# Kernel optimization log

Hardware: AMD Instinct MI355X
Metric: run time of the kernel (lower is better)

## Reference

```python
import jax, jax.numpy as jnp
from jax import lax
import numpy as np

NUM_LABELS = 48
BATCH, SEQ_LEN = 512, 1024


def setup_inputs() -> dict:
    key = jax.random.key(0)
    k1, k2, k3, k4, k5 = jax.random.split(key, 5)
    emissions = jax.random.normal(k1, (BATCH, SEQ_LEN, NUM_LABELS), dtype=jnp.float32)
    labels = jax.random.randint(k2, (BATCH, SEQ_LEN), 0, NUM_LABELS, dtype=jnp.int32)
    mask = jnp.ones((BATCH, SEQ_LEN), dtype=jnp.int32)
    transitions = jax.random.normal(k3, (NUM_LABELS, NUM_LABELS), dtype=jnp.float32)
    start_transitions = jax.random.normal(k4, (NUM_LABELS,), dtype=jnp.float32)
    end_transitions = jax.random.normal(k5, (NUM_LABELS,), dtype=jnp.float32)
    return {
        "emissions": emissions,
        "labels": labels,
        "mask": mask,
        "transitions": transitions,
        "start_transitions": start_transitions,
        "end_transitions": end_transitions,
    }


def _gold_score(emissions, labels, mask, transitions, start_transitions, end_transitions):
    maskf = mask.astype(emissions.dtype)
    # emissions gathered at gold labels: (B, T)
    emit = jnp.take_along_axis(emissions, labels[..., None], axis=2)[..., 0]
    # NOTE: original indexes transitions[labels_t, labels_{t-1}] (cur, prev)
    trans = transitions[labels[:, 1:], labels[:, :-1]]  # (B, T-1)
    lengths = jnp.sum(mask, axis=1) - 1  # index of last real token
    last_labels = jnp.take_along_axis(labels, lengths[:, None], axis=1)[:, 0]
    score = (start_transitions[labels[:, 0]] + emit[:, 0]
             + jnp.sum((emit[:, 1:] + trans) * maskf[:, 1:], axis=1)
             + end_transitions[last_labels])
    return score  # (B,)


def _forward_algorithm(emissions, mask, transitions, start_transitions, end_transitions):
    # carry: alpha scores (B, L)
    score0 = start_transitions[None, :] + emissions[:, 0]

    def step(score, xs):
        emit_t, mask_t = xs  # (B, L), (B,)
        # logsumexp over previous label i of score[b,i] + transitions[i,j]
        next_score = jax.nn.logsumexp(score[:, :, None] + transitions[None, :, :], axis=1) + emit_t
        score = jnp.where(mask_t[:, None].astype(bool), next_score, score)
        return score, None

    xs = (jnp.moveaxis(emissions[:, 1:], 1, 0), jnp.moveaxis(mask[:, 1:], 1, 0))
    score, _ = lax.scan(step, score0, xs)
    return jax.nn.logsumexp(score + end_transitions[None, :], axis=1)  # (B,)


def reference(emissions, labels, mask, transitions, start_transitions, end_transitions):
    gold = _gold_score(emissions, labels, mask, transitions, start_transitions, end_transitions)
    fwd = _forward_algorithm(emissions, mask, transitions, start_transitions, end_transitions)
    return jnp.mean(fwd - gold)
```

## Files before the change

### kernel.cpp

```cpp
#include <hip/hip_runtime.h>

constexpr int NL    = 48;
constexpr int SEQ   = 1024;
constexpr int BATCH = 512;

__device__ __forceinline__ float lane_bcast(float v, int lane) {
    return __int_as_float(__builtin_amdgcn_readlane(__float_as_int(v), lane));
}

#define CRF_STEP(T_, SLOT_, RN_) do {                                         \
    float ee_ = __expf(embuf[SLOT_]);                                         \
    int   mt_ = mbuf[SLOT_];                                                  \
    int   tn_ = (T_) + 8; if (tn_ > SEQ - 1) tn_ = SEQ - 1;                   \
    embuf[SLOT_] = em[tn_ * NL + jc];                                         \
    mbuf[SLOT_]  = mk[tn_];                                                   \
    float sv_[NL];                                                            \
    _Pragma("unroll")                                                         \
    for (int i_ = 0; i_ < NL; ++i_) sv_[i_] = lane_bcast(v, i_);              \
    float rm_ = 1.0f;                                                         \
    if (RN_) {                                                                \
        unsigned um_ = __float_as_uint(sv_[0]);                               \
        _Pragma("unroll")                                                     \
        for (int i_ = 1; i_ < NL; ++i_) {                                     \
            unsigned u2_ = __float_as_uint(sv_[i_]);                          \
            um_ = (um_ > u2_) ? um_ : u2_;                                    \
        }                                                                     \
        float m_ = __uint_as_float(um_);                                      \
        rm_ = __builtin_amdgcn_rcpf(m_);                                      \
        S += __logf(m_);                                                      \
    }                                                                         \
    float a0_ = 0.f, a1_ = 0.f, a2_ = 0.f, a3_ = 0.f;                         \
    _Pragma("unroll")                                                         \
    for (int i_ = 0; i_ < NL; i_ += 4) {                                      \
        a0_ = fmaf(sv_[i_ + 0], Ec[i_ + 0], a0_);                             \
        a1_ = fmaf(sv_[i_ + 1], Ec[i_ + 1], a1_);                             \
        a2_ = fmaf(sv_[i_ + 2], Ec[i_ + 2], a2_);                             \
        a3_ = fmaf(sv_[i_ + 3], Ec[i_ + 3], a3_);                             \
    }                                                                         \
    float acc_ = (a0_ + a1_) + (a2_ + a3_);                                   \
    v = (mt_ ? acc_ * ee_ : v) * rm_;                                         \
} while (0)

__global__ __launch_bounds__(128)
__attribute__((amdgpu_waves_per_eu(1, 1)))
void crf_fused(
    const float* __restrict__ emissions, const int* __restrict__ labels,
    const int* __restrict__ mask, const float* __restrict__ trans,
    const float* __restrict__ startt, const float* __restrict__ endt,
    float* __restrict__ gold_out, float* __restrict__ fwd_out)
{
    const int b   = blockIdx.x;
    const int tid = threadIdx.x;
    const float* em = emissions + (size_t)b * SEQ * NL;
    const int*   mk = mask + b * SEQ;

    if (tid < 64) {
        const int  j   = tid;
        const bool act = (j < NL);
        const int  jc  = act ? j : NL - 1;

        float Ec[NL];
        #pragma unroll
        for (int i = 0; i < NL; ++i) Ec[i] = __expf(trans[i * NL + jc]);

        float s0 = act ? (startt[jc] + em[jc]) : -3.0e38f;
        float m0 = s0;
        #pragma unroll
        for (int o = 32; o; o >>= 1) m0 = fmaxf(m0, __shfl_xor(m0, o));
        float v = act ? __expf(s0 - m0) : 0.0f;
        float S = m0;

        float embuf[8]; int mbuf[8];
        #pragma unroll
        for (int t = 1; t <= 8; ++t) { embuf[t & 7] = em[t * NL + jc]; mbuf[t & 7] = mk[t]; }

        CRF_STEP(1, 1, 0); CRF_STEP(2, 2, 0); CRF_STEP(3, 3, 0); CRF_STEP(4, 4, 0);
        CRF_STEP(5, 5, 1); CRF_STEP(6, 6, 0); CRF_STEP(7, 7, 0);

        for (int tb = 8; tb <= SEQ - 8; tb += 8) {
            CRF_STEP(tb + 0, 0, 1);
            CRF_STEP(tb + 1, 1, 0); CRF_STEP(tb + 2, 2, 0); CRF_STEP(tb + 3, 3, 0);
            CRF_STEP(tb + 4, 4, 1);
            CRF_STEP(tb + 5, 5, 0); CRF_STEP(tb + 6, 6, 0); CRF_STEP(tb + 7, 7, 0);
        }

        float w = act ? v * __expf(endt[jc]) : 0.0f;
        #pragma unroll
        for (int o = 32; o; o >>= 1) w += __shfl_xor(w, o);
        if (j == 0) fwd_out[b] = S + __logf(w);
    } else {
        const int l = tid - 64;
        const int* lb = labels + b * SEQ;

        float part = 0.0f; int mcnt = 0;
        for (int t = l; t < SEQ; t += 64) {
            int lt = lb[t];
            int mt = mk[t];
            mcnt += mt;
            if (t == 0) {
                part += startt[lt] + em[lt];
            } else {
                float e  = em[t * NL + lt];
                float tr = trans[lt * NL + lb[t - 1]];
                if (mt) part += e + tr;
            }
        }
        #pragma unroll
        for (int o = 32; o; o >>= 1) {
            part += __shfl_xor(part, o);
            mcnt += __shfl_xor(mcnt, o);
        }
        if (l == 0) {
            int len = mcnt - 1;
            gold_out[b] = part + endt[lb[len]];
        }
    }
}

__global__ __launch_bounds__(64) void crf_reduce(
    const float* __restrict__ gold, const float* __restrict__ fwd,
    float* __restrict__ out)
{
    const int l = threadIdx.x;
    float s = 0.0f;
    for (int bIdx = l; bIdx < BATCH; bIdx += 64) s += fwd[bIdx] - gold[bIdx];
    #pragma unroll
    for (int o = 32; o; o >>= 1) s += __shfl_xor(s, o);
    if (l == 0) out[0] = s * (1.0f / (float)BATCH);
}

extern "C" void kernel_launch(void* const* d_in, const int* in_sizes, int n_in,
                              void* d_out, int out_size, void* d_ws, size_t ws_size,
                              hipStream_t stream) {
    const float* emissions = (const float*)d_in[0];
    const int*   labels    = (const int*)d_in[1];
    const int*   mask      = (const int*)d_in[2];
    const float* trans     = (const float*)d_in[3];
    const float* startt    = (const float*)d_in[4];
    const float* endt      = (const float*)d_in[5];
    float*       out       = (float*)d_out;
    float*       wsf       = (float*)d_ws;

    crf_fused<<<BATCH, 128, 0, stream>>>(emissions, labels, mask, trans, startt, endt,
                                         wsf, wsf + BATCH);
    crf_reduce<<<1, 64, 0, stream>>>(wsf, wsf + BATCH, out);
}
```

Before: 356.2 us.

## Pack alpha into bf16 pairs to halve readlane broadcasts per CRF step

Each step now rounds every lane's alpha to bf16, pairs neighbouring lanes with a DPP swap, and packs two bf16 values into one 32-bit word. Only 24 readlanes are needed per step instead of 48, and the values are unpacked into floats in scalar/vector ALU before the FMAs. The aim is to shorten the serial readlane chain on the recurrence's critical path. In exchange, the carried probabilities lose precision to bf16 across 1024 steps, which may affect accuracy, and the extra shift and mask operations add ALU work.

```diff
diff --git a/kernel.cpp b/kernel.cpp
--- a/kernel.cpp
+++ b/kernel.cpp
@@ -3,10 +3,6 @@
 constexpr int NL    = 48;
 constexpr int SEQ   = 1024;
 constexpr int BATCH = 512;
-
-__device__ __forceinline__ float lane_bcast(float v, int lane) {
-    return __int_as_float(__builtin_amdgcn_readlane(__float_as_int(v), lane));
-}
 
 #define CRF_STEP(T_, SLOT_, RN_) do {                                         \
     float ee_ = __expf(embuf[SLOT_]);                                         \
@@ -14,28 +10,42 @@
     int   tn_ = (T_) + 8; if (tn_ > SEQ - 1) tn_ = SEQ - 1;                   \
     embuf[SLOT_] = em[tn_ * NL + jc];                                         \
     mbuf[SLOT_]  = mk[tn_];                                                   \
-    float sv_[NL];                                                            \
+    int ar_ = __float_as_int(v) + 0x8000;          \
+    int br_ = __builtin_amdgcn_update_dpp(0, ar_, 0xB1, 0xF, 0xF, false);     \
+    int xl_ = odd ? br_ : ar_;                   \
+    int xh_ = odd ? ar_ : br_;                   \
+    int pk_ = (int)(((unsigned)xl_ >> 16) | ((unsigned)xh_ & 0xFFFF0000u));   \
+    int sp_[24];                                                              \
     _Pragma("unroll")                                                         \
-    for (int i_ = 0; i_ < NL; ++i_) sv_[i_] = lane_bcast(v, i_);              \
+    for (int p_ = 0; p_ < 24; ++p_)                                           \
+        sp_[p_] = __builtin_amdgcn_readlane(pk_, 2 * p_);                     \
     float rm_ = 1.0f;                                                         \
     if (RN_) {                                                                \
-        unsigned um_ = __float_as_uint(sv_[0]);                               \
+        unsigned mh_ = 0u, ml_ = 0u;                                          \
         _Pragma("unroll")                                                     \
-        for (int i_ = 1; i_ < NL; ++i_) {                                     \
-            unsigned u2_ = __float_as_uint(sv_[i_]);                          \
-            um_ = (um_ > u2_) ? um_ : u2_;                                    \
+        for (int p_ = 0; p_ < 24; ++p_) {                                     \
+            unsigned u_ = (unsigned)sp_[p_];                                  \
+            mh_ = (mh_ > u_) ? mh_ : u_;                                      \
+            unsigned l_ = u_ << 16;                                           \
+            ml_ = (ml_ > l_) ? ml_ : l_;                                      \
         }                                                                     \
-        float m_ = __uint_as_float(um_);                                      \
+        mh_ &= 0xFFFF0000u;                                                   \
+        unsigned mb_ = (mh_ > ml_) ? mh_ : ml_;                               \
+        float m_ = __uint_as_float(mb_);                                      \
         rm_ = __builtin_amdgcn_rcpf(m_);                                      \
         S += __logf(m_);                                                      \
     }                                                                         \
     float a0_ = 0.f, a1_ = 0.f, a2_ = 0.f, a3_ = 0.f;                         \
     _Pragma("unroll")                                                         \
-    for (int i_ = 0; i_ < NL; i_ += 4) {                                      \
-        a0_ = fmaf(sv_[i_ + 0], Ec[i_ + 0], a0_);                             \
-        a1_ = fmaf(sv_[i_ + 1], Ec[i_ + 1], a1_);                             \
-        a2_ = fmaf(sv_[i_ + 2], Ec[i_ + 2], a2_);                             \
-        a3_ = fmaf(sv_[i_ + 3], Ec[i_ + 3], a3_);                             \
+    for (int p_ = 0; p_ < 24; p_ += 2) {                                      \
+        float l0_ = __int_as_float((int)((unsigned)sp_[p_]     << 16));       \
+        float h0_ = __int_as_float((int)((unsigned)sp_[p_]     & 0xFFFF0000u));\
+        float l1_ = __int_as_float((int)((unsigned)sp_[p_ + 1] << 16));       \
+        float h1_ = __int_as_float((int)((unsigned)sp_[p_ + 1] & 0xFFFF0000u));\
+        a0_ = fmaf(l0_, Ec[2 * p_ + 0], a0_);                                 \
+        a1_ = fmaf(h0_, Ec[2 * p_ + 1], a1_);                                 \
+        a2_ = fmaf(l1_, Ec[2 * p_ + 2], a2_);                                 \
+        a3_ = fmaf(h1_, Ec[2 * p_ + 3], a3_);                                 \
     }                                                                         \
     float acc_ = (a0_ + a1_) + (a2_ + a3_);                                   \
     v = (mt_ ? acc_ * ee_ : v) * rm_;                                         \
@@ -58,6 +68,7 @@
         const int  j   = tid;
         const bool act = (j < NL);
         const int  jc  = act ? j : NL - 1;
+        const bool odd = (j & 1);
 
         float Ec[NL];
         #pragma unroll
```

Measured after the change: 412.3 us. +15.7%, slower.

## Interleave two batch sequences per wavefront to expose ILP in the CRF recurrence

Applied to the files above, without the earlier changes.

Each block now runs the forward recurrence for two batch elements (b and b+BATCH/2) inside one wavefront. The two independent chains are interleaved at each step: readlane broadcasts, max-renormalisation and FMAs for both are grouped in chunks of eight. The grid is halved to BATCH/2 blocks, and the gold-score wave loops over both sequences. The aim is to hide readlane and FMA latency on the serial dependency chain, at the cost of half as many concurrently active waves, more instructions per wave and higher register pressure.

```diff
diff --git a/kernel.cpp b/kernel.cpp
--- a/kernel.cpp
+++ b/kernel.cpp
@@ -8,37 +8,56 @@
     return __int_as_float(__builtin_amdgcn_readlane(__float_as_int(v), lane));
 }
 
-#define CRF_STEP(T_, SLOT_, RN_) do {                                         \
-    float ee_ = __expf(embuf[SLOT_]);                                         \
-    int   mt_ = mbuf[SLOT_];                                                  \
+#define CRF_STEP2(T_, SLOT_, RN_) do {                                        \
+    float eeA_ = __expf(embufA[SLOT_]);                                       \
+    float eeB_ = __expf(embufB[SLOT_]);                                       \
+    int   mtA_ = mbufA[SLOT_], mtB_ = mbufB[SLOT_];                           \
     int   tn_ = (T_) + 8; if (tn_ > SEQ - 1) tn_ = SEQ - 1;                   \
-    embuf[SLOT_] = em[tn_ * NL + jc];                                         \
-    mbuf[SLOT_]  = mk[tn_];                                                   \
-    float sv_[NL];                                                            \
+    embufA[SLOT_] = emA[tn_ * NL + jc];  mbufA[SLOT_] = mkA[tn_];             \
+    embufB[SLOT_] = emB[tn_ * NL + jc];  mbufB[SLOT_] = mkB[tn_];             \
+    float a0_=0.f,a1_=0.f,a2_=0.f,a3_=0.f;                                    \
+    float b0_=0.f,b1_=0.f,b2_=0.f,b3_=0.f;                                    \
+    unsigned umA_ = 0u, umB_ = 0u;                                            \
     _Pragma("unroll")                                                         \
-    for (int i_ = 0; i_ < NL; ++i_) sv_[i_] = lane_bcast(v, i_);              \
-    float rm_ = 1.0f;                                                         \
+    for (int g_ = 0; g_ < NL; g_ += 8) {                                      \
+        float sA_[8], sB_[8];                                                 \
+        _Pragma("unroll")                                                     \
+        for (int k_ = 0; k_ < 8; ++k_) {                                      \
+            sA_[k_] = lane_bcast(vA, g_ + k_);                                \
+            sB_[k_] = lane_bcast(vB, g_ + k_);                                \
+        }                                                                     \
+        if (RN_) {                                                            \
+            _Pragma("unroll")                                                 \
+            for (int k_ = 0; k_ < 8; ++k_) {                                  \
+                unsigned uA_ = __float_as_uint(sA_[k_]);                      \
+                umA_ = (umA_ > uA_) ? umA_ : uA_;                             \
+                unsigned uB_ = __float_as_uint(sB_[k_]);                      \
+                umB_ = (umB_ > uB_) ? umB_ : uB_;                             \
+            }                                                                 \
+        }                                                                     \
+        _Pragma("unroll")                                                     \
+        for (int k_ = 0; k_ < 8; k_ += 4) {                                   \
+            a0_ = fmaf(sA_[k_+0], Ec[g_+k_+0], a0_);                          \
+            b0_ = fmaf(sB_[k_+0], Ec[g_+k_+0], b0_);                          \
+            a1_ = fmaf(sA_[k_+1], Ec[g_+k_+1], a1_);                          \
+            b1_ = fmaf(sB_[k_+1], Ec[g_+k_+1], b1_);                          \
+            a2_ = fmaf(sA_[k_+2], Ec[g_+k_+2], a2_);                          \
+            b2_ = fmaf(sB_[k_+2], Ec[g_+k_+2], b2_);                          \
+            a3_ = fmaf(sA_[k_+3], Ec[g_+k_+3], a3_);                          \
+            b3_ = fmaf(sB_[k_+3], Ec[g_+k_+3], b3_);                          \
+        }                                                                     \
+    }                                                                         \
+    float rmA_ = 1.0f, rmB_ = 1.0f;                                           \
     if (RN_) {                                                                \
-        unsigned um_ = __float_as_uint(sv_[0]);                               \
-        _Pragma("unroll")                                                     \
-        for (int i_ = 1; i_ < NL; ++i_) {                                     \
-            unsigned u2_ = __float_as_uint(sv_[i_]);                          \
-            um_ = (um_ > u2_) ? um_ : u2_;                                    \
-        }                                                                     \
-        float m_ = __uint_as_float(um_);                                      \
-        rm_ = __builtin_amdgcn_rcpf(m_);                                      \
-        S += __logf(m_);                                                      \
+        float mA_ = __uint_as_float(umA_);                                    \
+        float mB_ = __uint_as_float(umB_);                                    \
+        rmA_ = __builtin_amdgcn_rcpf(mA_);  SA += __logf(mA_);                \
+        rmB_ = __builtin_amdgcn_rcpf(mB_);  SB += __logf(mB_);                \
     }                                                                         \
-    float a0_ = 0.f, a1_ = 0.f, a2_ = 0.f, a3_ = 0.f;                         \
-    _Pragma("unroll")                                                         \
-    for (int i_ = 0; i_ < NL; i_ += 4) {                                      \
-        a0_ = fmaf(sv_[i_ + 0], Ec[i_ + 0], a0_);                             \
-        a1_ = fmaf(sv_[i_ + 1], Ec[i_ + 1], a1_);                             \
-        a2_ = fmaf(sv_[i_ + 2], Ec[i_ + 2], a2_);                             \
-        a3_ = fmaf(sv_[i_ + 3], Ec[i_ + 3], a3_);                             \
-    }                                                                         \
-    float acc_ = (a0_ + a1_) + (a2_ + a3_);                                   \
-    v = (mt_ ? acc_ * ee_ : v) * rm_;                                         \
+    float accA_ = (a0_ + a1_) + (a2_ + a3_);                                  \
+    float accB_ = (b0_ + b1_) + (b2_ + b3_);                                  \
+    vA = (mtA_ ? accA_ * eeA_ : vA) * rmA_;                                   \
+    vB = (mtB_ ? accB_ * eeB_ : vB) * rmB_;                                   \
 } while (0)
 
 __global__ __launch_bounds__(128)
@@ -49,70 +68,97 @@
     const float* __restrict__ startt, const float* __restrict__ endt,
     float* __restrict__ gold_out, float* __restrict__ fwd_out)
 {
-    const int b   = blockIdx.x;
+    const int bA  = blockIdx.x;
+    const int bB  = blockIdx.x + (BATCH / 2);
     const int tid = threadIdx.x;
-    const float* em = emissions + (size_t)b * SEQ * NL;
-    const int*   mk = mask + b * SEQ;
 
     if (tid < 64) {
         const int  j   = tid;
         const bool act = (j < NL);
         const int  jc  = act ? j : NL - 1;
 
+        const float* emA = emissions + (size_t)bA * SEQ * NL;
+        const float* emB = emissions + (size_t)bB * SEQ * NL;
+        const int*   mkA = mask + bA * SEQ;
+        const int*   mkB = mask + bB * SEQ;
+
         float Ec[NL];
         #pragma unroll
         for (int i = 0; i < NL; ++i) Ec[i] = __expf(trans[i * NL + jc]);
 
-        float s0 = act ? (startt[jc] + em[jc]) : -3.0e38f;
-        float m0 = s0;
+        float st_ = act ? startt[jc] : 0.0f;
+        float s0A = act ? (st_ + emA[jc]) : -3.0e38f;
+        float s0B = act ? (st_ + emB[jc]) : -3.0e38f;
+        float m0A = s0A, m0B = s0B;
         #pragma unroll
-        for (int o = 32; o; o >>= 1) m0 = fmaxf(m0, __shfl_xor(m0, o));
-        float v = act ? __expf(s0 - m0) : 0.0f;
-        float S = m0;
+        for (int o = 32; o; o >>= 1) {
+            m0A = fmaxf(m0A, __shfl_xor(m0A, o));
+            m0B = fmaxf(m0B, __shfl_xor(m0B, o));
+        }
+        float vA = act ? __expf(s0A - m0A) : 0.0f;
+        float vB = act ? __expf(s0B - m0B) : 0.0f;
+        float SA = m0A, SB = m0B;
 
-        float embuf[8]; int mbuf[8];
+        float embufA[8], embufB[8]; int mbufA[8], mbufB[8];
         #pragma unroll
-        for (int t = 1; t <= 8; ++t) { embuf[t & 7] = em[t * NL + jc]; mbuf[t & 7] = mk[t]; }
+        for (int t = 1; t <= 8; ++t) {
+            embufA[t & 7] = emA[t * NL + jc];  mbufA[t & 7] = mkA[t];
+            embufB[t & 7] = emB[t * NL + jc];  mbufB[t & 7] = mkB[t];
+        }
 
-        CRF_STEP(1, 1, 0); CRF_STEP(2, 2, 0); CRF_STEP(3, 3, 0); CRF_STEP(4, 4, 0);
-        CRF_STEP(5, 5, 1); CRF_STEP(6, 6, 0); CRF_STEP(7, 7, 0);
+        CRF_STEP2(1, 1, 0); CRF_STEP2(2, 2, 0); CRF_STEP2(3, 3, 0); CRF_STEP2(4, 4, 0);
+        CRF_STEP2(5, 5, 1); CRF_STEP2(6, 6, 0); CRF_STEP2(7, 7, 0);
 
         for (int tb = 8; tb <= SEQ - 8; tb += 8) {
-            CRF_STEP(tb + 0, 0, 1);
-            CRF_STEP(tb + 1, 1, 0); CRF_STEP(tb + 2, 2, 0); CRF_STEP(tb + 3, 3, 0);
-            CRF_STEP(tb + 4, 4, 1);
-            CRF_STEP(tb + 5, 5, 0); CRF_STEP(tb + 6, 6, 0); CRF_STEP(tb + 7, 7, 0);
+            CRF_STEP2(tb + 0, 0, 1);
+            CRF_STEP2(tb + 1, 1, 0); CRF_STEP2(tb + 2, 2, 0); CRF_STEP2(tb + 3, 3, 0);
+            CRF_STEP2(tb + 4, 4, 1);
+            CRF_STEP2(tb + 5, 5, 0); CRF_STEP2(tb + 6, 6, 0); CRF_STEP2(tb + 7, 7, 0);
         }
 
-        float w = act ? v * __expf(endt[jc]) : 0.0f;
+        float ed_ = act ? __expf(endt[jc]) : 0.0f;
+        float wA = act ? vA * ed_ : 0.0f;
+        float wB = act ? vB * ed_ : 0.0f;
         #pragma unroll
-        for (int o = 32; o; o >>= 1) w += __shfl_xor(w, o);
-        if (j == 0) fwd_out[b] = S + __logf(w);
+        for (int o = 32; o; o >>= 1) {
+            wA += __shfl_xor(wA, o);
+            wB += __shfl_xor(wB, o);
+        }
+        if (j == 0) {
+            fwd_out[bA] = SA + __logf(wA);
+            fwd_out[bB] = SB + __logf(wB);
+        }
     } else {
         const int l = tid - 64;
-        const int* lb = labels + b * SEQ;
+        #pragma unroll
+        for (int c = 0; c < 2; ++c) {
+            const int bb = (c == 0) ? bA : bB;
+            const int*   lb = labels + bb * SEQ;
+            const int*   mk = mask + bb * SEQ;
+            const float* em = emissions + (size_t)bb * SEQ * NL;
 
-        float part = 0.0f; int mcnt = 0;
-        for (int t = l; t < SEQ; t += 64) {
-            int lt = lb[t];
-            int mt = mk[t];
-            mcnt += mt;
-            if (t == 0) {
-                part += startt[lt] + em[lt];
-            } else {
-                float e  = em[t * NL + lt];
-                float tr = trans[lt * NL + lb[t - 1]];
-                if (mt) part += e + tr;
+            float part = 0.0f; int mcnt = 0;
+            for (int t = l; t < SEQ; t += 64) {
+                int lt = lb[t];
+                int mt = mk[t];
+                mcnt += mt;
+                if (t == 0) {
+                    part += startt[lt] + em[lt];
+                } else {
+                    float e  = em[t * NL + lt];
+                    float tr = trans[lt * NL + lb[t - 1]];
+                    if (mt) part += e + tr;
+                }
             }
-        }
-        #pragma unroll
-        for (int o = 32; o; o >>= 1) {
-            part += __shfl_xor(part, o);
-            mcnt += __shfl_xor(mcnt, o);
-        }
-        if (l == 0) {
-            int len = mcnt - 1;
-            gold_out[b] = part + endt[lb[len]];
+            #pragma unroll
+            for (int o = 32; o; o >>= 1) {
+                part += __shfl_xor(part, o);
+                mcnt += __shfl_xor(mcnt, o);
+            }
+            if (l == 0) {
+                int len = mcnt - 1;
+                gold_out[bb] = part + endt[lb[len]];
+            }
         }
     }
 }
@@ -141,7 +187,7 @@
     float*       out       = (float*)d_out;
     float*       wsf       = (float*)d_ws;
 
-    crf_fused<<<BATCH, 128, 0, stream>>>(emissions, labels, mask, trans, startt, endt,
-                                         wsf, wsf + BATCH);
+    crf_fused<<<BATCH / 2, 128, 0, stream>>>(emissions, labels, mask, trans,
+                                             startt, endt, wsf, wsf + BATCH);
     crf_reduce<<<1, 64, 0, stream>>>(wsf, wsf + BATCH, out);
 }
```

Measured after the change: 537.5 us. 1.51x slower.

## Batch 16 sequences per wave and run CRF forward recursion on bf16 MFMA

Applied to the files above, without the earlier changes.

The forward recursion now handles 16 batch rows per wavefront and computes each step's 48x48 exp-domain matrix-vector product as bf16 MFMA 16x16x32 instructions. The alpha vector goes through LDS in bf16 between steps, replacing the 48 readlane broadcasts and scalar FMAs per lane. Gold-score work is moved to separate blocks covering 8 rows each, and the grid shrinks to 32 forward blocks plus 64 gold blocks. This cuts per-step instruction count but runs on only 32 CUs, adds an LDS round-trip per step, and lowers the precision of transitions and alpha to bf16.

```diff
diff --git a/kernel.cpp b/kernel.cpp
--- a/kernel.cpp
+++ b/kernel.cpp
@@ -3,45 +3,72 @@
 constexpr int NL    = 48;
 constexpr int SEQ   = 1024;
 constexpr int BATCH = 512;
-
-__device__ __forceinline__ float lane_bcast(float v, int lane) {
-    return __int_as_float(__builtin_amdgcn_readlane(__float_as_int(v), lane));
-}
-
-#define CRF_STEP(T_, SLOT_, RN_) do {                                         \
-    float ee_ = __expf(embuf[SLOT_]);                                         \
-    int   mt_ = mbuf[SLOT_];                                                  \
-    int   tn_ = (T_) + 8; if (tn_ > SEQ - 1) tn_ = SEQ - 1;                   \
-    embuf[SLOT_] = em[tn_ * NL + jc];                                         \
-    mbuf[SLOT_]  = mk[tn_];                                                   \
-    float sv_[NL];                                                            \
-    _Pragma("unroll")                                                         \
-    for (int i_ = 0; i_ < NL; ++i_) sv_[i_] = lane_bcast(v, i_);              \
+constexpr int FWDB  = 32;
+constexpr int LSTR  = 72;
+
+typedef short bf16x8 __attribute__((ext_vector_type(8)));
+typedef float f32x4  __attribute__((ext_vector_type(4)));
+
+__device__ __forceinline__ unsigned short bf16r(float x) {
+    unsigned u = __float_as_uint(x);
+    u += 0x7FFFu + ((u >> 16) & 1u);
+    return (unsigned short)(u >> 16);
+}
+__device__ __forceinline__ unsigned bf16pk(float a, float b) {
+    unsigned ua = __float_as_uint(a); ua += 0x7FFFu + ((ua >> 16) & 1u);
+    unsigned ub = __float_as_uint(b); ub += 0x7FFFu + ((ub >> 16) & 1u);
+    return (ua >> 16) | (ub & 0xFFFF0000u);
+}
+
+#define STEP(T_, S_, RN_) do {                                                \
+    const int    mt_ = mring[S_];                                             \
+    const float4 e0_ = ering0[S_];                                            \
+    const float4 e1_ = ering1[S_];                                            \
+    const float4 e2_ = ering2[S_];                                            \
+    { int tn_ = (T_) + 4; if (tn_ > SEQ - 1) tn_ = SEQ - 1;                   \
+      ering0[S_] = *(const float4*)(emb + tn_ * NL + eoff0);                  \
+      ering1[S_] = *(const float4*)(emb + tn_ * NL + eoff1);                  \
+      ering2[S_] = *(const float4*)(emb + tn_ * NL + eoff2);                  \
+      mring[S_]  = mkb[tn_]; }                                                \
+    const bf16x8 bLo_ = *(const bf16x8*)&vb[rdLo];                            \
+    const bf16x8 bHi_ = *(const bf16x8*)&vb[rdHi];                            \
+    f32x4 d0_ = {0.f, 0.f, 0.f, 0.f};                                         \
+    f32x4 d1_ = {0.f, 0.f, 0.f, 0.f};                                         \
+    f32x4 d2_ = {0.f, 0.f, 0.f, 0.f};                                         \
+    d0_ = __builtin_amdgcn_mfma_f32_16x16x32_bf16(aL[0], bLo_, d0_, 0, 0, 0); \
+    d1_ = __builtin_amdgcn_mfma_f32_16x16x32_bf16(aL[1], bLo_, d1_, 0, 0, 0); \
+    d2_ = __builtin_amdgcn_mfma_f32_16x16x32_bf16(aL[2], bLo_, d2_, 0, 0, 0); \
+    d0_ = __builtin_amdgcn_mfma_f32_16x16x32_bf16(aH[0], bHi_, d0_, 0, 0, 0); \
+    d1_ = __builtin_amdgcn_mfma_f32_16x16x32_bf16(aH[1], bHi_, d1_, 0, 0, 0); \
+    d2_ = __builtin_amdgcn_mfma_f32_16x16x32_bf16(aH[2], bHi_, d2_, 0, 0, 0); \
     float rm_ = 1.0f;                                                         \
     if (RN_) {                                                                \
-        unsigned um_ = __float_as_uint(sv_[0]);                               \
-        _Pragma("unroll")                                                     \
-        for (int i_ = 1; i_ < NL; ++i_) {                                     \
-            unsigned u2_ = __float_as_uint(sv_[i_]);                          \
-            um_ = (um_ > u2_) ? um_ : u2_;                                    \
-        }                                                                     \
-        float m_ = __uint_as_float(um_);                                      \
-        rm_ = __builtin_amdgcn_rcpf(m_);                                      \
-        S += __logf(m_);                                                      \
+        float mx_ = fmaxf(fmaxf(fmaxf(vc0[0], vc0[1]), fmaxf(vc0[2], vc0[3])),\
+                          fmaxf(fmaxf(vc1[0], vc1[1]), fmaxf(vc1[2], vc1[3])));\
+        mx_ = fmaxf(mx_, fmaxf(fmaxf(vc2[0], vc2[1]), fmaxf(vc2[2], vc2[3]))); \
+        mx_ = fmaxf(mx_, __shfl_xor(mx_, 16));                                \
+        mx_ = fmaxf(mx_, __shfl_xor(mx_, 32));                                \
+        rm_ = __builtin_amdgcn_rcpf(mx_);                                     \
+        S  += __logf(mx_);                                                    \
     }                                                                         \
-    float a0_ = 0.f, a1_ = 0.f, a2_ = 0.f, a3_ = 0.f;                         \
-    _Pragma("unroll")                                                         \
-    for (int i_ = 0; i_ < NL; i_ += 4) {                                      \
-        a0_ = fmaf(sv_[i_ + 0], Ec[i_ + 0], a0_);                             \
-        a1_ = fmaf(sv_[i_ + 1], Ec[i_ + 1], a1_);                             \
-        a2_ = fmaf(sv_[i_ + 2], Ec[i_ + 2], a2_);                             \
-        a3_ = fmaf(sv_[i_ + 3], Ec[i_ + 3], a3_);                             \
-    }                                                                         \
-    float acc_ = (a0_ + a1_) + (a2_ + a3_);                                   \
-    v = (mt_ ? acc_ * ee_ : v) * rm_;                                         \
+    vc0[0] = (mt_ ? d0_[0] * __expf(e0_.x) : vc0[0]) * rm_;                   \
+    vc0[1] = (mt_ ? d0_[1] * __expf(e0_.y) : vc0[1]) * rm_;                   \
+    vc0[2] = (mt_ ? d0_[2] * __expf(e0_.z) : vc0[2]) * rm_;                   \
+    vc0[3] = (mt_ ? d0_[3] * __expf(e0_.w) : vc0[3]) * rm_;                   \
+    vc1[0] = (mt_ ? d1_[0] * __expf(e1_.x) : vc1[0]) * rm_;                   \
+    vc1[1] = (mt_ ? d1_[1] * __expf(e1_.y) : vc1[1]) * rm_;                   \
+    vc1[2] = (mt_ ? d1_[2] * __expf(e1_.z) : vc1[2]) * rm_;                   \
+    vc1[3] = (mt_ ? d1_[3] * __expf(e1_.w) : vc1[3]) * rm_;                   \
+    vc2[0] = (mt_ ? d2_[0] * __expf(e2_.x) : vc2[0]) * rm_;                   \
+    vc2[1] = (mt_ ? d2_[1] * __expf(e2_.y) : vc2[1]) * rm_;                   \
+    vc2[2] = (mt_ ? d2_[2] * __expf(e2_.z) : vc2[2]) * rm_;                   \
+    vc2[3] = (mt_ ? d2_[3] * __expf(e2_.w) : vc2[3]) * rm_;                   \
+    *(uint2*)&vb[wr0] = make_uint2(bf16pk(vc0[0], vc0[1]), bf16pk(vc0[2], vc0[3])); \
+    *(uint2*)&vb[wr1] = make_uint2(bf16pk(vc1[0], vc1[1]), bf16pk(vc1[2], vc1[3])); \
+    *(uint2*)&vb[wr2] = make_uint2(bf16pk(vc2[0], vc2[1]), bf16pk(vc2[2], vc2[3])); \
 } while (0)
 
-__global__ __launch_bounds__(128)
+__global__ __launch_bounds__(256)
 __attribute__((amdgpu_waves_per_eu(1, 1)))
 void crf_fused(
     const float* __restrict__ emissions, const int* __restrict__ labels,
@@ -49,70 +76,129 @@
     const float* __restrict__ startt, const float* __restrict__ endt,
     float* __restrict__ gold_out, float* __restrict__ fwd_out)
 {
-    const int b   = blockIdx.x;
+    __shared__ __align__(16) unsigned short vb[16 * LSTR];
     const int tid = threadIdx.x;
-    const float* em = emissions + (size_t)b * SEQ * NL;
-    const int*   mk = mask + b * SEQ;
-
-    if (tid < 64) {
-        const int  j   = tid;
-        const bool act = (j < NL);
-        const int  jc  = act ? j : NL - 1;
-
-        float Ec[NL];
-        #pragma unroll
-        for (int i = 0; i < NL; ++i) Ec[i] = __expf(trans[i * NL + jc]);
-
-        float s0 = act ? (startt[jc] + em[jc]) : -3.0e38f;
-        float m0 = s0;
-        #pragma unroll
-        for (int o = 32; o; o >>= 1) m0 = fmaxf(m0, __shfl_xor(m0, o));
-        float v = act ? __expf(s0 - m0) : 0.0f;
-        float S = m0;
-
-        float embuf[8]; int mbuf[8];
-        #pragma unroll
-        for (int t = 1; t <= 8; ++t) { embuf[t & 7] = em[t * NL + jc]; mbuf[t & 7] = mk[t]; }
-
-        CRF_STEP(1, 1, 0); CRF_STEP(2, 2, 0); CRF_STEP(3, 3, 0); CRF_STEP(4, 4, 0);
-        CRF_STEP(5, 5, 1); CRF_STEP(6, 6, 0); CRF_STEP(7, 7, 0);
-
-        for (int tb = 8; tb <= SEQ - 8; tb += 8) {
-            CRF_STEP(tb + 0, 0, 1);
-            CRF_STEP(tb + 1, 1, 0); CRF_STEP(tb + 2, 2, 0); CRF_STEP(tb + 3, 3, 0);
-            CRF_STEP(tb + 4, 4, 1);
-            CRF_STEP(tb + 5, 5, 0); CRF_STEP(tb + 6, 6, 0); CRF_STEP(tb + 7, 7, 0);
-        }
-
-        float w = act ? v * __expf(endt[jc]) : 0.0f;
-        #pragma unroll
-        for (int o = 32; o; o >>= 1) w += __shfl_xor(w, o);
-        if (j == 0) fwd_out[b] = S + __logf(w);
+
+    if (blockIdx.x < FWDB) {
+        if (tid >= 64) return;
+        const int L  = tid;
+        const int n  = L & 15;
+        const int q  = L >> 4;
+        const int bt = blockIdx.x;
+        const int bn = 16 * bt + n;
+
+        const float* emb = emissions + (size_t)bn * SEQ * NL;
+        const int*   mkb = mask + bn * SEQ;
+
+        const int eoff0 = 4 * q, eoff1 = 16 + 4 * q, eoff2 = 32 + 4 * q;
+        const int rdLo = LSTR * n + 8 * q;
+        const int rdHi = rdLo + 32;
+        const int wr0  = LSTR * n + 4 * q;
+        const int wr1  = wr0 + 16;
+        const int wr2  = wr0 + 32;
+
+        bf16x8 aL[3], aH[3];
+        #pragma unroll
+        for (int mt = 0; mt < 3; ++mt) {
+            #pragma unroll
+            for (int j = 0; j < 8; ++j) {
+                int kL = 8 * q + j;
+                aL[mt][j] = (short)bf16r(__expf(trans[kL * NL + 16 * mt + n]));
+                int kH = 32 + 8 * q + j;
+                int idx = (kH < NL) ? (kH * NL + 16 * mt + n) : 0;
+                float tv = trans[idx];
+                aH[mt][j] = (kH < NL) ? (short)bf16r(__expf(tv)) : (short)0;
+            }
+        }
+
+        for (int i = L; i < 16 * LSTR; i += 64) vb[i] = 0;
+
+        float s_[12];
+        #pragma unroll
+        for (int mt = 0; mt < 3; ++mt)
+            #pragma unroll
+            for (int r = 0; r < 4; ++r) {
+                int c = 16 * mt + 4 * q + r;
+                s_[mt * 4 + r] = startt[c] + emb[c];
+            }
+        float mx = s_[0];
+        #pragma unroll
+        for (int i = 1; i < 12; ++i) mx = fmaxf(mx, s_[i]);
+        mx = fmaxf(mx, __shfl_xor(mx, 16));
+        mx = fmaxf(mx, __shfl_xor(mx, 32));
+        float S = mx;
+        f32x4 vc0, vc1, vc2;
+        #pragma unroll
+        for (int r = 0; r < 4; ++r) {
+            vc0[r] = __expf(s_[r]     - mx);
+            vc1[r] = __expf(s_[4 + r] - mx);
+            vc2[r] = __expf(s_[8 + r] - mx);
+        }
+        *(uint2*)&vb[wr0] = make_uint2(bf16pk(vc0[0], vc0[1]), bf16pk(vc0[2], vc0[3]));
+        *(uint2*)&vb[wr1] = make_uint2(bf16pk(vc1[0], vc1[1]), bf16pk(vc1[2], vc1[3]));
+        *(uint2*)&vb[wr2] = make_uint2(bf16pk(vc2[0], vc2[1]), bf16pk(vc2[2], vc2[3]));
+
+        float4 ering0[4], ering1[4], ering2[4]; int mring[4];
+        #pragma unroll
+        for (int t = 1; t <= 4; ++t) {
+            int s = t & 3;
+            ering0[s] = *(const float4*)(emb + t * NL + eoff0);
+            ering1[s] = *(const float4*)(emb + t * NL + eoff1);
+            ering2[s] = *(const float4*)(emb + t * NL + eoff2);
+            mring[s]  = mkb[t];
+        }
+
+        STEP(1, 1, 0); STEP(2, 2, 0); STEP(3, 3, 0);
+        for (int tb = 4; tb <= SEQ - 4; tb += 4) {
+            STEP(tb + 0, 0, 1);
+            STEP(tb + 1, 1, 0); STEP(tb + 2, 2, 0); STEP(tb + 3, 3, 0);
+        }
+
+        float w = 0.0f;
+        #pragma unroll
+        for (int mt = 0; mt < 3; ++mt)
+            #pragma unroll
+            for (int r = 0; r < 4; ++r) {
+                int c = 16 * mt + 4 * q + r;
+                float vv = (mt == 0) ? vc0[r] : (mt == 1) ? vc1[r] : vc2[r];
+                w += vv * __expf(endt[c]);
+            }
+        w += __shfl_xor(w, 16);
+        w += __shfl_xor(w, 32);
+        if (q == 0) fwd_out[bn] = S + __logf(w);
     } else {
-        const int l = tid - 64;
-        const int* lb = labels + b * SEQ;
-
-        float part = 0.0f; int mcnt = 0;
-        for (int t = l; t < SEQ; t += 64) {
-            int lt = lb[t];
-            int mt = mk[t];
-            mcnt += mt;
-            if (t == 0) {
-                part += startt[lt] + em[lt];
-            } else {
-                float e  = em[t * NL + lt];
-                float tr = trans[lt * NL + lb[t - 1]];
-                if (mt) part += e + tr;
-            }
-        }
-        #pragma unroll
-        for (int o = 32; o; o >>= 1) {
-            part += __shfl_xor(part, o);
-            mcnt += __shfl_xor(mcnt, o);
-        }
-        if (l == 0) {
-            int len = mcnt - 1;
-            gold_out[b] = part + endt[lb[len]];
+        const int gb = blockIdx.x - FWDB;
+        const int wv = tid >> 6;
+        const int l  = tid & 63;
+        #pragma unroll
+        for (int c = 0; c < 2; ++c) {
+            const int bb = gb * 8 + wv * 2 + c;
+            const int*   lb = labels + bb * SEQ;
+            const int*   mk = mask + bb * SEQ;
+            const float* em = emissions + (size_t)bb * SEQ * NL;
+
+            float part = 0.0f; int mcnt = 0;
+            for (int t = l; t < SEQ; t += 64) {
+                int lt = lb[t];
+                int mt = mk[t];
+                mcnt += mt;
+                if (t == 0) {
+                    part += startt[lt] + em[lt];
+                } else {
+                    float e  = em[t * NL + lt];
+                    float tr = trans[lt * NL + lb[t - 1]];
+                    if (mt) part += e + tr;
+                }
+            }
+            #pragma unroll
+            for (int o = 32; o; o >>= 1) {
+                part += __shfl_xor(part, o);
+                mcnt += __shfl_xor(mcnt, o);
+            }
+            if (l == 0) {
+                int len = mcnt - 1;
+                gold_out[bb] = part + endt[lb[len]];
+            }
         }
     }
 }
@@ -141,7 +227,7 @@
     float*       out       = (float*)d_out;
     float*       wsf       = (float*)d_ws;
 
-    crf_fused<<<BATCH, 128, 0, stream>>>(emissions, labels, mask, trans, startt, endt,
-                                         wsf, wsf + BATCH);
+    crf_fused<<<FWDB + 64, 256, 0, stream>>>(emissions, labels, mask, trans,
+                                             startt, endt, wsf, wsf + BATCH);
     crf_reduce<<<1, 64, 0, stream>>>(wsf, wsf + BATCH, out);
 }
```

After: 521.1 us. +46.3%, slower.
